# Kernel optimization log

Measured on AMD Instinct MI355X. Metric: run time of the kernel, lower is better.

Reference implementation:

```python
import jax, jax.numpy as jnp
import numpy as np

B, A, D = 512, 32, 256      # batch clips, actors (nodes per graph), feature dim
E = 1048576                 # total edges over the flattened (B*A)-node graph
THRESHOLD = 0.5             # config.knn.threshold
EPS = 1e-5


def setup_inputs() -> dict:
    key = jax.random.key(0)
    k1, k2, k3 = jax.random.split(key, 3)
    N = B * A
    X = jax.random.normal(k1, (B, A, D), dtype=jnp.float32)
    edge_index = jax.random.randint(k2, (2, E), 0, N, dtype=jnp.int32)
    W = jax.random.normal(k3, (D, D), dtype=jnp.float32) * (1.0 / np.sqrt(D))
    b = jnp.zeros((D,), dtype=jnp.float32)
    return {"X": X, "edge_index": edge_index, "W": W, "b": b}


def gcn_conv(x, edge_index, W, b):
    # Standard GCNConv: x' = D^-1/2 (A + I) D^-1/2 (x W) + b
    N = x.shape[0]
    x = x @ W                                            # [N, D]
    loop = jnp.arange(N, dtype=edge_index.dtype)
    src = jnp.concatenate([edge_index[0], loop])         # message sources
    tgt = jnp.concatenate([edge_index[1], loop])         # aggregation targets
    deg = jax.ops.segment_sum(jnp.ones_like(src, dtype=x.dtype), tgt,
                              num_segments=N)            # in-degree incl. self-loop
    dinv = jnp.where(deg > 0, jax.lax.rsqrt(deg), 0.0)
    coef = (dinv[src] * dinv[tgt])[:, None]              # symmetric norm per edge
    out = jax.ops.segment_sum(x[src] * coef, tgt, num_segments=N)
    return out + b


def reference(X, edge_index, W, b):
    Bq, Aq, Dq = X.shape
    x = X.reshape(Bq * Aq, Dq)
    x = gcn_conv(x, edge_index, W, b)
    Xo = x.reshape(Bq, Aq, Dq)

    # cal_edge: pairwise squared distances per batch, min-max normalized,
    # thresholded. Instead of variable-length dense_to_sparse edge lists we
    # return the equivalent fixed-shape adjacency mask [B, A, A].
    inner = -2.0 * jnp.einsum('bad,bcd->bac', Xo, Xo)
    sq = jnp.sum(Xo * Xo, axis=-1, keepdims=True)        # [B, A, 1]
    scores = sq + inner + jnp.swapaxes(sq, -1, -2)       # [B, A, A]
    smin = scores.min(axis=-1, keepdims=True)
    smax = scores.max(axis=-1, keepdims=True)
    scores = (scores - smin) / (smax - smin + EPS)
    adj_mask = scores > THRESHOLD                        # new edge set (dense form)
    return Xo, adj_mask
```

## Files before the change

### kernel.cpp

```cpp
#include <hip/hip_runtime.h>

#define BQ 512
#define AQ 32
#define DQ 256
#define NQ (BQ * AQ)
#define EQ 1048576
#define THR 0.5f
#define EPSF 1e-5f
#define DEG_STRIDE 160
#define BIN_TGTS 64
#define NBINS (NQ / BIN_TGTS)
#define BIN_STRIDE 4864

typedef __attribute__((ext_vector_type(8))) short bf16x8;
typedef __attribute__((ext_vector_type(4))) float f32x4;

__device__ __forceinline__ unsigned short f2bf(float f) {
    unsigned int u = __float_as_uint(f);
    return (unsigned short)((u + 0x7FFFu + ((u >> 16) & 1u)) >> 16);
}
__device__ __forceinline__ float bf2f(unsigned short h) {
    return __uint_as_float((unsigned int)h << 16);
}

__global__ __launch_bounds__(256) void k_wt_part(
        const float* __restrict__ W, unsigned short* __restrict__ Wt,
        const int* __restrict__ src, const int* __restrict__ tgt,
        int* __restrict__ bin_cursor, unsigned int* __restrict__ binned) {
    __shared__ int hist[NBINS];
    int tid = threadIdx.x;
    if (blockIdx.x < 256) {
        int idx = blockIdx.x * 256 + tid;
        int n = idx >> 8;
        int k = idx & 255;
        float w = W[k * DQ + n];
        unsigned short h = f2bf(w);
        Wt[idx] = h;
        Wt[DQ * DQ + idx] = f2bf(w - bf2f(h));
        return;
    }
    hist[tid] = 0;
    __syncthreads();
    int base = (blockIdx.x - 256) * 4096;
    int t[16], s[16];
    #pragma unroll
    for (int i = 0; i < 16; i++) {
        int e = base + i * 256 + tid;
        t[i] = tgt[e];
        s[i] = src[e];
        atomicAdd(&hist[t[i] >> 6], 1);
    }
    __syncthreads();
    int mine = hist[tid];
    __syncthreads();
    hist[tid] = tid * BIN_STRIDE + atomicAdd(&bin_cursor[tid], mine);
    __syncthreads();
    #pragma unroll
    for (int i = 0; i < 16; i++) {
        int slot = atomicAdd(&hist[t[i] >> 6], 1);
        binned[slot] = ((unsigned int)t[i] << 14) | (unsigned int)s[i];
    }
}

__global__ __launch_bounds__(256) void k_gemm_cnt(
        const float* __restrict__ Xp, const unsigned short* __restrict__ Wt,
        unsigned short* __restrict__ xwb,
        const int* __restrict__ bin_cursor, const unsigned int* __restrict__ binned,
        float* __restrict__ dinv) {
    __shared__ unsigned short bs[2][256 * 40];
    int tid = threadIdx.x;
    if (blockIdx.x >= 256) {
        int* lcnt = (int*)&bs[0][0];
        int b = blockIdx.x - 256;
        if (tid < BIN_TGTS) lcnt[tid] = 0;
        __syncthreads();
        int beg = b * BIN_STRIDE;
        int count = bin_cursor[b];
        if (count > BIN_STRIDE) count = BIN_STRIDE;
        for (int i = beg + tid; i < beg + count; i += 256) {
            unsigned int ed = binned[i];
            atomicAdd(&lcnt[(ed >> 14) & 63], 1);
        }
        __syncthreads();
        if (tid < BIN_TGTS)
            dinv[b * BIN_TGTS + tid] = rsqrtf((float)(lcnt[tid] + 1));
        return;
    }
    int wave = tid >> 6;
    int lane = tid & 63;
    int col = lane & 15;
    int quad = lane >> 4;
    int mbase = blockIdx.x * 64 + wave * 16;
    int m = mbase + col;

    const float* arow = Xp + (size_t)m * DQ;
    const unsigned short* Wlo = Wt + DQ * DQ;

    f32x4 acc[16];
    f32x4 zero = {0.f, 0.f, 0.f, 0.f};
    #pragma unroll
    for (int i = 0; i < 16; i++) acc[i] = zero;

    for (int k0 = 0; k0 < DQ; k0 += 32) {
        __syncthreads();
        {
            const uint4* gh = (const uint4*)(Wt + tid * DQ + k0);
            const uint4* gl = (const uint4*)(Wlo + tid * DQ + k0);
            uint4* lh = (uint4*)&bs[0][tid * 40];
            uint4* ll = (uint4*)&bs[1][tid * 40];
            #pragma unroll
            for (int u = 0; u < 4; u++) lh[u] = gh[u];
            #pragma unroll
            for (int u = 0; u < 4; u++) ll[u] = gl[u];
        }
        __syncthreads();

        int kq = k0 + quad * 8;
        float4 a0 = *(const float4*)(arow + kq);
        float4 a1 = *(const float4*)(arow + kq + 4);
        float av[8] = {a0.x, a0.y, a0.z, a0.w, a1.x, a1.y, a1.z, a1.w};
        bf16x8 ah, al;
        #pragma unroll
        for (int j = 0; j < 8; j++) {
            unsigned short h = f2bf(av[j]);
            ah[j] = (short)h;
            al[j] = (short)f2bf(av[j] - bf2f(h));
        }
        #pragma unroll
        for (int nt = 0; nt < 16; nt++) {
            int n = nt * 16 + col;
            bf16x8 bh = *(const bf16x8*)&bs[0][n * 40 + quad * 8];
            bf16x8 bl = *(const bf16x8*)&bs[1][n * 40 + quad * 8];
            acc[nt] = __builtin_amdgcn_mfma_f32_16x16x32_bf16(ah, bh, acc[nt], 0, 0, 0);
            acc[nt] = __builtin_amdgcn_mfma_f32_16x16x32_bf16(al, bh, acc[nt], 0, 0, 0);
            acc[nt] = __builtin_amdgcn_mfma_f32_16x16x32_bf16(ah, bl, acc[nt], 0, 0, 0);
        }
    }

    #pragma unroll
    for (int nt = 0; nt < 16; nt++) {
        #pragma unroll
        for (int r = 0; r < 4; r++) {
            xwb[(size_t)(mbase + quad * 4 + r) * DQ + nt * 16 + col] =
                f2bf(acc[nt][r]);
        }
    }
}

__global__ __launch_bounds__(512) void k_agg_scores(
        const unsigned int* __restrict__ xwb,
        const unsigned int* __restrict__ binned,
        const int* __restrict__ bin_cursor,
        const float* __restrict__ dinv,
        const float* __restrict__ bias,
        float* __restrict__ out,
        float* __restrict__ mask) {
    __shared__ float xs[AQ][DQ + 4];
    __shared__ float sq[AQ];
    __shared__ float sc[AQ][AQ + 1];
    __shared__ float rmin[AQ], rmax[AQ];
    __shared__ unsigned short lbuck[AQ * DEG_STRIDE];
    __shared__ int lcnt[AQ];

    int tid = threadIdx.x;
    int wave = tid >> 6;
    int lane = tid & 63;
    int bq = blockIdx.x;
    const uint2* xw2 = (const uint2*)xwb;

    if (tid < AQ) lcnt[tid] = 0;
    __syncthreads();
    {
        int b = bq >> 1;
        int beg = b * BIN_STRIDE;
        int count = bin_cursor[b];
        if (count > BIN_STRIDE) count = BIN_STRIDE;
        for (int i = beg + tid; i < beg + count; i += 512) {
            unsigned int ed = binned[i];
            if ((int)(ed >> 19) == bq) {
                int a = (ed >> 14) & 31;
                int pos = atomicAdd(&lcnt[a], 1);
                if (pos < DEG_STRIDE)
                    lbuck[a * DEG_STRIDE + pos] = (unsigned short)(ed & 0x3FFFu);
            }
        }
    }
    __syncthreads();

    float4 bv = ((const float4*)bias)[lane];

    #pragma unroll 1
    for (int i = 0; i < 4; i++) {
        int a = wave * 4 + i;
        int t = bq * AQ + a;
        float dt = dinv[t];
        float c0 = dt * dt;
        uint2 sp = xw2[(size_t)t * 64 + lane];
        float4 acc;
        acc.x = __uint_as_float(sp.x << 16) * c0;
        acc.y = __uint_as_float(sp.x & 0xFFFF0000u) * c0;
        acc.z = __uint_as_float(sp.y << 16) * c0;
        acc.w = __uint_as_float(sp.y & 0xFFFF0000u) * c0;

        int num = lcnt[a];
        if (num > DEG_STRIDE) num = DEG_STRIDE;
        for (int k0 = 0; k0 < num; k0 += 64) {
            int rem = num - k0;
            int n = rem < 64 ? rem : 64;
            int idx = k0 + (lane < n ? lane : 0);
            int e = (int)lbuck[a * DEG_STRIDE + idx];
            float cl = (lane < n) ? dinv[e] * dt : 0.f;
            int n8 = (n + 7) & ~7;
            for (int j0 = 0; j0 < n8; j0 += 8) {
                #pragma unroll
                for (int jj = 0; jj < 8; jj++) {
                    int j = j0 + jj;
                    int s = __shfl(e, j);
                    float c = __shfl(cl, j);
                    uint2 p = xw2[(size_t)s * 64 + lane];
                    acc.x += __uint_as_float(p.x << 16) * c;
                    acc.y += __uint_as_float(p.x & 0xFFFF0000u) * c;
                    acc.z += __uint_as_float(p.y << 16) * c;
                    acc.w += __uint_as_float(p.y & 0xFFFF0000u) * c;
                }
            }
        }

        acc.x += bv.x; acc.y += bv.y; acc.z += bv.z; acc.w += bv.w;
        ((float4*)out)[(size_t)t * 64 + lane] = acc;
        *(float4*)&xs[a][lane * 4] = acc;
    }
    __syncthreads();

    if (tid < AQ) {
        const float4* xi = (const float4*)xs[tid];
        float s = 0.f;
        #pragma unroll 8
        for (int dd = 0; dd < DQ / 4; dd++) {
            float4 a = xi[dd];
            s += a.x * a.x + a.y * a.y + a.z * a.z + a.w * a.w;
        }
        sq[tid] = s;
    }
    __syncthreads();

    {
        int p0 = tid * 2;
        int i = p0 >> 5;
        int j0 = p0 & 31;
        const float4* xi = (const float4*)xs[i];
        float g[2] = {0.f, 0.f};
        for (int dd = 0; dd < DQ / 4; dd += 8) {
            float4 ar[8];
            #pragma unroll
            for (int u = 0; u < 8; u++) ar[u] = xi[dd + u];
            #pragma unroll
            for (int q = 0; q < 2; q++) {
                const float4* xj = (const float4*)xs[j0 + q];
                float gq = 0.f;
                #pragma unroll
                for (int u = 0; u < 8; u++) {
                    float4 b = xj[dd + u];
                    gq += ar[u].x * b.x + ar[u].y * b.y +
                          ar[u].z * b.z + ar[u].w * b.w;
                }
                g[q] += gq;
            }
        }
        #pragma unroll
        for (int q = 0; q < 2; q++) {
            sc[i][j0 + q] = sq[i] - 2.f * g[q] + sq[j0 + q];
        }
    }
    __syncthreads();

    if (tid < AQ) {
        float mn = sc[tid][0], mx = sc[tid][0];
        for (int j = 1; j < AQ; j++) {
            float v = sc[tid][j];
            mn = fminf(mn, v);
            mx = fmaxf(mx, v);
        }
        rmin[tid] = mn;
        rmax[tid] = mx;
    }
    __syncthreads();

    {
        float* mb = mask + (size_t)bq * AQ * AQ;
        int p0 = tid * 2;
        int i = p0 >> 5, j0 = p0 & 31;
        float inv = 1.0f / (rmax[i] - rmin[i] + EPSF);
        float2 mv;
        mv.x = ((sc[i][j0 + 0] - rmin[i]) * inv > THR) ? 1.0f : 0.0f;
        mv.y = ((sc[i][j0 + 1] - rmin[i]) * inv > THR) ? 1.0f : 0.0f;
        ((float2*)mb)[tid] = mv;
    }
}

extern "C" void kernel_launch(void* const* d_in, const int* in_sizes, int n_in,
                              void* d_out, int out_size, void* d_ws, size_t ws_size,
                              hipStream_t stream) {
    const float* X    = (const float*)d_in[0];
    const int*   ei   = (const int*)d_in[1];
    const float* W    = (const float*)d_in[2];
    const float* bias = (const float*)d_in[3];
    float* out = (float*)d_out;

    char* ws = (char*)d_ws;
    unsigned short* xwb = (unsigned short*)ws;
    unsigned int* binned = (unsigned int*)(ws + (size_t)NQ * DQ * 2);
    unsigned short* Wt = (unsigned short*)(binned + (size_t)NBINS * BIN_STRIDE);
    float* dinv = (float*)(Wt + 2 * DQ * DQ);
    int* bin_cursor = (int*)(dinv + NQ);

    const int* src = ei;
    const int* tgt = ei + EQ;

    hipMemsetAsync(bin_cursor, 0, NBINS * sizeof(int), stream);
    k_wt_part<<<512, 256, 0, stream>>>(W, Wt, src, tgt, bin_cursor, binned);
    k_gemm_cnt<<<512, 256, 0, stream>>>(X, Wt, xwb, bin_cursor, binned, dinv);
    k_agg_scores<<<BQ, 512, 0, stream>>>((const unsigned int*)xwb, binned,
                                         bin_cursor, dinv, bias, out,
                                         out + (size_t)NQ * DQ);
}
```

Before: 172.8 us.

## Split fused aggregate+scores kernel into separate gather and scores kernels

Splits the combined aggregation and distance-score kernel into a gather kernel launched with twice as many blocks, each handling half of a graph's 32 nodes, and a separate scores kernel that reloads the aggregated output from global memory. The aim is more parallelism and lower shared memory per block in the latency-bound gather phase, for better occupancy. The cost is an extra kernel launch, a global write-then-read of the output for the scores stage, and each binned edge range being scanned twice (once per half-block).

```diff
diff --git a/kernel.cpp b/kernel.cpp
--- a/kernel.cpp
+++ b/kernel.cpp
@@ -147,28 +147,24 @@
     }
 }
 
-__global__ __launch_bounds__(512) void k_agg_scores(
+__global__ __launch_bounds__(512) void k_gather(
         const unsigned int* __restrict__ xwb,
         const unsigned int* __restrict__ binned,
         const int* __restrict__ bin_cursor,
         const float* __restrict__ dinv,
         const float* __restrict__ bias,
-        float* __restrict__ out,
-        float* __restrict__ mask) {
-    __shared__ float xs[AQ][DQ + 4];
-    __shared__ float sq[AQ];
-    __shared__ float sc[AQ][AQ + 1];
-    __shared__ float rmin[AQ], rmax[AQ];
-    __shared__ unsigned short lbuck[AQ * DEG_STRIDE];
-    __shared__ int lcnt[AQ];
+        float* __restrict__ out) {
+    __shared__ unsigned short lbuck[16 * DEG_STRIDE];
+    __shared__ int lcnt[16];
 
     int tid = threadIdx.x;
     int wave = tid >> 6;
     int lane = tid & 63;
-    int bq = blockIdx.x;
+    int bq = blockIdx.x >> 1;
+    int half = blockIdx.x & 1;
     const uint2* xw2 = (const uint2*)xwb;
 
-    if (tid < AQ) lcnt[tid] = 0;
+    if (tid < 16) lcnt[tid] = 0;
     __syncthreads();
     {
         int b = bq >> 1;
@@ -179,9 +175,12 @@
             unsigned int ed = binned[i];
             if ((int)(ed >> 19) == bq) {
                 int a = (ed >> 14) & 31;
-                int pos = atomicAdd(&lcnt[a], 1);
-                if (pos < DEG_STRIDE)
-                    lbuck[a * DEG_STRIDE + pos] = (unsigned short)(ed & 0x3FFFu);
+                if ((a >> 4) == half) {
+                    int al = a & 15;
+                    int pos = atomicAdd(&lcnt[al], 1);
+                    if (pos < DEG_STRIDE)
+                        lbuck[al * DEG_STRIDE + pos] = (unsigned short)(ed & 0x3FFFu);
+                }
             }
         }
     }
@@ -190,8 +189,9 @@
     float4 bv = ((const float4*)bias)[lane];
 
     #pragma unroll 1
-    for (int i = 0; i < 4; i++) {
-        int a = wave * 4 + i;
+    for (int i = 0; i < 2; i++) {
+        int al = wave * 2 + i;
+        int a = half * 16 + al;
         int t = bq * AQ + a;
         float dt = dinv[t];
         float c0 = dt * dt;
@@ -202,13 +202,13 @@
         acc.z = __uint_as_float(sp.y << 16) * c0;
         acc.w = __uint_as_float(sp.y & 0xFFFF0000u) * c0;
 
-        int num = lcnt[a];
+        int num = lcnt[al];
         if (num > DEG_STRIDE) num = DEG_STRIDE;
         for (int k0 = 0; k0 < num; k0 += 64) {
             int rem = num - k0;
             int n = rem < 64 ? rem : 64;
             int idx = k0 + (lane < n ? lane : 0);
-            int e = (int)lbuck[a * DEG_STRIDE + idx];
+            int e = (int)lbuck[al * DEG_STRIDE + idx];
             float cl = (lane < n) ? dinv[e] * dt : 0.f;
             int n8 = (n + 7) & ~7;
             for (int j0 = 0; j0 < n8; j0 += 8) {
@@ -228,7 +228,27 @@
 
         acc.x += bv.x; acc.y += bv.y; acc.z += bv.z; acc.w += bv.w;
         ((float4*)out)[(size_t)t * 64 + lane] = acc;
-        *(float4*)&xs[a][lane * 4] = acc;
+    }
+}
+
+__global__ __launch_bounds__(512) void k_scores(
+        const float* __restrict__ out,
+        float* __restrict__ mask) {
+    __shared__ float xs[AQ][DQ + 4];
+    __shared__ float sq[AQ];
+    __shared__ float sc[AQ][AQ + 1];
+    __shared__ float rmin[AQ], rmax[AQ];
+
+    int tid = threadIdx.x;
+    int bq = blockIdx.x;
+
+    {
+        int row = tid >> 4;
+        int seg = tid & 15;
+        const float4* g = (const float4*)(out + ((size_t)(bq * AQ + row)) * DQ + seg * 16);
+        float4* l = (float4*)&xs[row][seg * 16];
+        #pragma unroll
+        for (int u = 0; u < 4; u++) l[u] = g[u];
     }
     __syncthreads();
 
@@ -320,7 +340,7 @@
     hipMemsetAsync(bin_cursor, 0, NBINS * sizeof(int), stream);
     k_wt_part<<<512, 256, 0, stream>>>(W, Wt, src, tgt, bin_cursor, binned);
     k_gemm_cnt<<<512, 256, 0, stream>>>(X, Wt, xwb, bin_cursor, binned, dinv);
-    k_agg_scores<<<BQ, 512, 0, stream>>>((const unsigned int*)xwb, binned,
-                                         bin_cursor, dinv, bias, out,
-                                         out + (size_t)NQ * DQ);
-}
+    k_gather<<<2 * BQ, 512, 0, stream>>>((const unsigned int*)xwb, binned,
+                                         bin_cursor, dinv, bias, out);
+    k_scores<<<BQ, 512, 0, stream>>>(out, out + (size_t)NQ * DQ);
+}
```

After: 182.0 us. 1.05x slower.

## Replace global atomic edge bins with per-block sorted segments and offset tables

Applied to the files above, without the earlier changes.

The partition kernel now does a per-block prefix scan over bin counts, sorts its 4096 edges into shared memory by bin, and writes them out contiguously with coalesced stores. Per-block count and offset tables replace the global atomic bin cursors and the fixed-capacity bins, which also removes the memset and the overflow clamp. Consumers now walk 256 small segments per bin with per-thread serial loops. This trades global atomics and scattered writes for strided, less coalesced reads in the degree and aggregation stages.

```diff
diff --git a/kernel.cpp b/kernel.cpp
--- a/kernel.cpp
+++ b/kernel.cpp
@@ -10,7 +10,8 @@
 #define DEG_STRIDE 160
 #define BIN_TGTS 64
 #define NBINS (NQ / BIN_TGTS)
-#define BIN_STRIDE 4864
+#define NBLK_P 256
+#define EPB (EQ / NBLK_P)
 
 typedef __attribute__((ext_vector_type(8))) short bf16x8;
 typedef __attribute__((ext_vector_type(4))) float f32x4;
@@ -26,8 +27,12 @@
 __global__ __launch_bounds__(256) void k_wt_part(
         const float* __restrict__ W, unsigned short* __restrict__ Wt,
         const int* __restrict__ src, const int* __restrict__ tgt,
-        int* __restrict__ bin_cursor, unsigned int* __restrict__ binned) {
+        int* __restrict__ cntT, int* __restrict__ offT,
+        unsigned int* __restrict__ binned) {
+    __shared__ unsigned int buf[EPB];
     __shared__ int hist[NBINS];
+    __shared__ int sdat[NBINS];
+    __shared__ int cur[NBINS];
     int tid = threadIdx.x;
     if (blockIdx.x < 256) {
         int idx = blockIdx.x * 256 + tid;
@@ -39,9 +44,10 @@
         Wt[DQ * DQ + idx] = f2bf(w - bf2f(h));
         return;
     }
+    int blk = blockIdx.x - 256;
     hist[tid] = 0;
     __syncthreads();
-    int base = (blockIdx.x - 256) * 4096;
+    int base = blk * EPB;
     int t[16], s[16];
     #pragma unroll
     for (int i = 0; i < 16; i++) {
@@ -51,21 +57,37 @@
         atomicAdd(&hist[t[i] >> 6], 1);
     }
     __syncthreads();
-    int mine = hist[tid];
-    __syncthreads();
-    hist[tid] = tid * BIN_STRIDE + atomicAdd(&bin_cursor[tid], mine);
+    int v = hist[tid];
+    sdat[tid] = v;
+    __syncthreads();
+    #pragma unroll
+    for (int off = 1; off < 256; off <<= 1) {
+        int add = (tid >= off) ? sdat[tid - off] : 0;
+        __syncthreads();
+        sdat[tid] += add;
+        __syncthreads();
+    }
+    int excl = sdat[tid] - v;
+    cur[tid] = excl;
+    cntT[blk * NBINS + tid] = v;
+    offT[blk * NBINS + tid] = excl;
     __syncthreads();
     #pragma unroll
     for (int i = 0; i < 16; i++) {
-        int slot = atomicAdd(&hist[t[i] >> 6], 1);
-        binned[slot] = ((unsigned int)t[i] << 14) | (unsigned int)s[i];
-    }
+        int pos = atomicAdd(&cur[t[i] >> 6], 1);
+        buf[pos] = ((unsigned int)t[i] << 14) | (unsigned int)s[i];
+    }
+    __syncthreads();
+    unsigned int* g = binned + (size_t)blk * EPB;
+    #pragma unroll
+    for (int i = 0; i < 16; i++) g[i * 256 + tid] = buf[i * 256 + tid];
 }
 
 __global__ __launch_bounds__(256) void k_gemm_cnt(
         const float* __restrict__ Xp, const unsigned short* __restrict__ Wt,
         unsigned short* __restrict__ xwb,
-        const int* __restrict__ bin_cursor, const unsigned int* __restrict__ binned,
+        const int* __restrict__ cntT, const int* __restrict__ offT,
+        const unsigned int* __restrict__ binned,
         float* __restrict__ dinv) {
     __shared__ unsigned short bs[2][256 * 40];
     int tid = threadIdx.x;
@@ -74,13 +96,11 @@
         int b = blockIdx.x - 256;
         if (tid < BIN_TGTS) lcnt[tid] = 0;
         __syncthreads();
-        int beg = b * BIN_STRIDE;
-        int count = bin_cursor[b];
-        if (count > BIN_STRIDE) count = BIN_STRIDE;
-        for (int i = beg + tid; i < beg + count; i += 256) {
-            unsigned int ed = binned[i];
-            atomicAdd(&lcnt[(ed >> 14) & 63], 1);
-        }
+        int c = cntT[tid * NBINS + b];
+        int o = offT[tid * NBINS + b];
+        const unsigned int* e = binned + (size_t)tid * EPB + o;
+        for (int j = 0; j < c; j++)
+            atomicAdd(&lcnt[(e[j] >> 14) & 63], 1);
         __syncthreads();
         if (tid < BIN_TGTS)
             dinv[b * BIN_TGTS + tid] = rsqrtf((float)(lcnt[tid] + 1));
@@ -150,7 +170,7 @@
 __global__ __launch_bounds__(512) void k_agg_scores(
         const unsigned int* __restrict__ xwb,
         const unsigned int* __restrict__ binned,
-        const int* __restrict__ bin_cursor,
+        const int* __restrict__ cntT, const int* __restrict__ offT,
         const float* __restrict__ dinv,
         const float* __restrict__ bias,
         float* __restrict__ out,
@@ -172,11 +192,13 @@
     __syncthreads();
     {
         int b = bq >> 1;
-        int beg = b * BIN_STRIDE;
-        int count = bin_cursor[b];
-        if (count > BIN_STRIDE) count = BIN_STRIDE;
-        for (int i = beg + tid; i < beg + count; i += 512) {
-            unsigned int ed = binned[i];
+        int blk = tid & 255;
+        int half = tid >> 8;
+        int c = cntT[blk * NBINS + b];
+        int o = offT[blk * NBINS + b];
+        const unsigned int* ebase = binned + (size_t)blk * EPB + o;
+        for (int j = half; j < c; j += 2) {
+            unsigned int ed = ebase[j];
             if ((int)(ed >> 19) == bq) {
                 int a = (ed >> 14) & 31;
                 int pos = atomicAdd(&lcnt[a], 1);
@@ -310,17 +332,17 @@
     char* ws = (char*)d_ws;
     unsigned short* xwb = (unsigned short*)ws;
     unsigned int* binned = (unsigned int*)(ws + (size_t)NQ * DQ * 2);
-    unsigned short* Wt = (unsigned short*)(binned + (size_t)NBINS * BIN_STRIDE);
+    unsigned short* Wt = (unsigned short*)(binned + (size_t)NBLK_P * EPB);
     float* dinv = (float*)(Wt + 2 * DQ * DQ);
-    int* bin_cursor = (int*)(dinv + NQ);
+    int* cntT = (int*)(dinv + NQ);
+    int* offT = cntT + NBLK_P * NBINS;
 
     const int* src = ei;
     const int* tgt = ei + EQ;
 
-    hipMemsetAsync(bin_cursor, 0, NBINS * sizeof(int), stream);
-    k_wt_part<<<512, 256, 0, stream>>>(W, Wt, src, tgt, bin_cursor, binned);
-    k_gemm_cnt<<<512, 256, 0, stream>>>(X, Wt, xwb, bin_cursor, binned, dinv);
+    k_wt_part<<<512, 256, 0, stream>>>(W, Wt, src, tgt, cntT, offT, binned);
+    k_gemm_cnt<<<512, 256, 0, stream>>>(X, Wt, xwb, cntT, offT, binned, dinv);
     k_agg_scores<<<BQ, 512, 0, stream>>>((const unsigned int*)xwb, binned,
-                                         bin_cursor, dinv, bias, out,
+                                         cntT, offT, dinv, bias, out,
                                          out + (size_t)NQ * DQ);
 }
```

Measured after the change: 174.2 us. About the same (+0.8%).
